# Optimization experiments

Hardware: AMD Instinct MI355X
Metric: run time of the kernel (lower is better)

Reference implementation:

```python
import jax, jax.numpy as jnp
import numpy as np

N = 50000        # nodes
E = 800000       # edges (before self-loops)
IN = 512         # in_channels
HEADS = 8        # 'head' arg: heads and per-head out dim of conv1
C1 = 8           # per-head channels of conv1 (== head)
OUT = 128        # out_channels of conv2
NEG_SLOPE = 0.2  # PyG GATConv leaky-relu slope


def _glorot(key, shape, fan_in):
    return jax.random.normal(key, shape, jnp.float32) * (1.0 / np.sqrt(fan_in))


def setup_inputs() -> dict:
    key = jax.random.key(0)
    ks = jax.random.split(key, 10)
    x = jax.random.normal(ks[0], (N, IN), jnp.float32)
    edge_index = jax.random.randint(ks[1], (2, E), 0, N, dtype=jnp.int32)
    # conv1: GATConv(IN, C1, heads=HEADS, concat=True)
    W1 = _glorot(ks[2], (IN, HEADS * C1), IN)
    att_src1 = _glorot(ks[3], (HEADS, C1), C1)
    att_dst1 = _glorot(ks[4], (HEADS, C1), C1)
    bias1 = jnp.zeros((HEADS * C1,), jnp.float32)
    # conv2: GATConv(HEADS*C1, OUT, heads=1, concat=False)
    W2 = _glorot(ks[5], (HEADS * C1, OUT), HEADS * C1)
    att_src2 = _glorot(ks[6], (1, OUT), OUT)
    att_dst2 = _glorot(ks[7], (1, OUT), OUT)
    bias2 = jnp.zeros((OUT,), jnp.float32)
    return {"x": x, "edge_index": edge_index,
            "W1": W1, "att_src1": att_src1, "att_dst1": att_dst1, "bias1": bias1,
            "W2": W2, "att_src2": att_src2, "att_dst2": att_dst2, "bias2": bias2}


def gat_conv(x, src, dst, W, a_src, a_dst, bias, heads, concat):
    """PyG GATConv (eval mode, dropout off). src/dst already include self-loops."""
    n = x.shape[0]
    h = (x @ W).reshape(n, heads, -1)                 # [N, H, C]
    s = (h * a_src[None]).sum(-1)                     # [N, H] alpha_src per node
    d = (h * a_dst[None]).sum(-1)                     # [N, H] alpha_dst per node
    alpha = jax.nn.leaky_relu(s[src] + d[dst], NEG_SLOPE)  # [E, H]
    # segment softmax over incoming edges of each destination node
    amax = jax.ops.segment_max(alpha, dst, num_segments=n)  # [N, H]
    amax = jnp.where(jnp.isfinite(amax), amax, 0.0)
    ea = jnp.exp(alpha - amax[dst])                   # [E, H]
    denom = jax.ops.segment_sum(ea, dst, num_segments=n)
    w = ea / (denom[dst] + 1e-16)                     # [E, H]
    msg = h[src] * w[..., None]                       # [E, H, C]
    out = jax.ops.segment_sum(msg, dst, num_segments=n)  # [N, H, C]
    out = out.reshape(n, -1) if concat else out.mean(axis=1)
    return out + bias


def reference(x, edge_index, W1, att_src1, att_dst1, bias1,
              W2, att_src2, att_dst2, bias2):
    n = x.shape[0]
    loop = jnp.arange(n, dtype=edge_index.dtype)      # PyG adds self-loops
    src = jnp.concatenate([edge_index[0], loop])
    dst = jnp.concatenate([edge_index[1], loop])
    h = jax.nn.elu(gat_conv(x, src, dst, W1, att_src1, att_dst1, bias1,
                            heads=HEADS, concat=True))
    out = jax.nn.elu(gat_conv(h, src, dst, W2, att_src2, att_dst2, bias2,
                              heads=1, concat=False))
    return out
```

## Files before the change

kernel.cpp:

```cpp
#include <hip/hip_runtime.h>

#define NEG_SLOPE 0.2f
#define CAP 128

typedef __attribute__((ext_vector_type(8))) short bf16x8;
typedef __attribute__((ext_vector_type(4))) float f32x4;

__device__ __forceinline__ float leaky(float v) {
    return v > 0.0f ? v : NEG_SLOPE * v;
}
__device__ __forceinline__ float elu(float v) {
    return v > 0.0f ? v : (__expf(v) - 1.0f);
}
__device__ __forceinline__ short f2b(float f) {
    return (short)((__float_as_uint(f) + 0x8000u) >> 16);
}
__device__ __forceinline__ float bf2f(unsigned short v) {
    return __uint_as_float(((unsigned)v) << 16);
}

__global__ void prep_k(const float* __restrict__ W1, const float* __restrict__ W2,
                       unsigned short* __restrict__ w1s, unsigned short* __restrict__ w2s,
                       int* __restrict__ wp, int N) {
    int i = blockIdx.x * 256 + threadIdx.x;
    if (i < N) wp[i] = 0;
    if (i < 512 * 64) {
        int k = i >> 6, n = i & 63;
        int kt = k >> 5, kk = k & 31;
        int nt = n >> 4, nn = n & 15;
        int lane = (kk >> 3) * 16 + nn, j = kk & 7;
        w1s[(((size_t)(kt * 4 + nt)) * 64 + lane) * 8 + j] = (unsigned short)f2b(W1[i]);
    } else if (i < 512 * 64 + 64 * 128) {
        int i2 = i - 512 * 64;
        int k = i2 >> 7, n = i2 & 127;
        int kt = k >> 5, kk = k & 31;
        int nt = n >> 4, nn = n & 15;
        int lane = (kk >> 3) * 16 + nn, j = kk & 7;
        w2s[(((size_t)(kt * 8 + nt)) * 64 + lane) * 8 + j] = (unsigned short)f2b(W2[i2]);
    }
}

__global__ __launch_bounds__(256) void g1pack_k(const float* __restrict__ X,
                                                const unsigned short* __restrict__ Ws,
                                                const float* __restrict__ Asrc,
                                                const float* __restrict__ Adst,
                                                unsigned short* __restrict__ Hb,
                                                float* __restrict__ S,
                                                float* __restrict__ D,
                                                const int* __restrict__ ei, int E,
                                                int* __restrict__ wp,
                                                int* __restrict__ srcs,
                                                int N, int gblk) {
    if ((int)blockIdx.x >= gblk) {
        int e = ((int)blockIdx.x - gblk) * 256 + threadIdx.x;
        if (e < E) {
            int s = ei[e];
            int d = ei[E + e];
            int c = atomicAdd(&wp[d], 1);
            if (c < CAP) srcs[((size_t)d << 7) + c] = s;
        }
        return;
    }
    const int lane = threadIdx.x & 63;
    const int wave = threadIdx.x >> 6;
    const int m0 = blockIdx.x * 64 + wave * 16;
    const int q = lane >> 4, lc = lane & 15;
    const int arow = m0 + lc;
    const float* xrow = X + (size_t)min(arow, N - 1) * 512 + q * 8;
    const bf16x8* bW = (const bf16x8*)Ws;

    f32x4 acc[4] = {{0.f,0.f,0.f,0.f},{0.f,0.f,0.f,0.f},{0.f,0.f,0.f,0.f},{0.f,0.f,0.f,0.f}};

    for (int g = 0; g < 2; ++g) {
        float4 a[16];
#pragma unroll
        for (int u = 0; u < 16; ++u)
            a[u] = *(const float4*)(xrow + g * 256 + (u >> 1) * 32 + (u & 1) * 4);
#pragma unroll
        for (int u2 = 0; u2 < 8; ++u2) {
            const int kt = g * 8 + u2;
            float4 a0 = a[u2 * 2], a1 = a[u2 * 2 + 1];
            bf16x8 af;
            af[0] = f2b(a0.x); af[1] = f2b(a0.y); af[2] = f2b(a0.z); af[3] = f2b(a0.w);
            af[4] = f2b(a1.x); af[5] = f2b(a1.y); af[6] = f2b(a1.z); af[7] = f2b(a1.w);
#pragma unroll
            for (int nt = 0; nt < 4; ++nt) {
                bf16x8 bf = bW[(size_t)(kt * 4 + nt) * 64 + lane];
                acc[nt] = __builtin_amdgcn_mfma_f32_16x16x32_bf16(af, bf, acc[nt], 0, 0, 0);
            }
        }
    }

    float asc[4], adc[4];
#pragma unroll
    for (int nt = 0; nt < 4; ++nt) { asc[nt] = Asrc[nt * 16 + lc]; adc[nt] = Adst[nt * 16 + lc]; }

#pragma unroll
    for (int r = 0; r < 4; ++r) {
        int row = m0 + q * 4 + r;
        bool ok = row < N;
        if (ok) {
#pragma unroll
            for (int nt = 0; nt < 4; ++nt)
                Hb[(size_t)row * 64 + nt * 16 + lc] = (unsigned short)f2b(acc[nt][r]);
        }
        float ps[4], pd[4];
#pragma unroll
        for (int nt = 0; nt < 4; ++nt) { ps[nt] = acc[nt][r] * asc[nt]; pd[nt] = acc[nt][r] * adc[nt]; }
#pragma unroll
        for (int off = 1; off < 8; off <<= 1) {
#pragma unroll
            for (int nt = 0; nt < 4; ++nt) {
                ps[nt] += __shfl_xor(ps[nt], off);
                pd[nt] += __shfl_xor(pd[nt], off);
            }
        }
        if (ok && !(lc & 7)) {
            int hb = lc >> 3;
#pragma unroll
            for (int nt = 0; nt < 4; ++nt) {
                S[(size_t)row * 8 + nt * 2 + hb] = ps[nt];
                D[(size_t)row * 8 + nt * 2 + hb] = pd[nt];
            }
        }
    }
}

__global__ __launch_bounds__(256) void agg1g2_k(const int* __restrict__ wp,
                                                const int* __restrict__ srcs,
                                                const float* __restrict__ S1,
                                                const float* __restrict__ D1,
                                                const unsigned short* __restrict__ H1b,
                                                const float* __restrict__ b1,
                                                const unsigned short* __restrict__ W2s,
                                                const float* __restrict__ as2,
                                                const float* __restrict__ ad2,
                                                unsigned short* __restrict__ H2b,
                                                float* __restrict__ S2,
                                                float* __restrict__ D2, int N) {
    __shared__ unsigned short sh[16][64];
    __shared__ float shp[4][16], shq[4][16];

    const int tid  = threadIdx.x;
    const int lane = tid & 63;
    const int wave = tid >> 6;
    const int m0 = blockIdx.x * 16;

    const int h = lane & 7;
    const int eg = lane >> 3;
#pragma unroll
    for (int rep = 0; rep < 4; ++rep) {
        const int nl = wave * 4 + rep;
        const int wid = m0 + nl;
        if (wid < N) {
            const int deg = min(wp[wid], CAP);
            const size_t b0 = (size_t)wid << 7;
            const float dvh = D1[(size_t)wid * 8 + h];

            float wself = __expf(leaky(S1[(size_t)wid * 8 + h] + dvh));
            float den = (eg == 0) ? wself : 0.0f;
            float acc[8] = {0.f,0.f,0.f,0.f,0.f,0.f,0.f,0.f};
            if (eg == 0) {
                bf16x8 hv = *(const bf16x8*)(H1b + (size_t)wid * 64 + h * 8);
#pragma unroll
                for (int c = 0; c < 8; ++c)
                    acc[c] = wself * bf2f((unsigned short)hv[c]);
            }

            for (int base = 0; base < deg; base += 8) {
                int i = base + eg;
                bool v = i < deg;
                int src = v ? srcs[b0 + i] : wid;
                float w = v ? __expf(leaky(S1[(size_t)src * 8 + h] + dvh)) : 0.0f;
                den += w;
                bf16x8 hv = *(const bf16x8*)(H1b + (size_t)src * 64 + h * 8);
#pragma unroll
                for (int c = 0; c < 8; ++c)
                    acc[c] += w * bf2f((unsigned short)hv[c]);
            }
#pragma unroll
            for (int off = 8; off < 64; off <<= 1) {
                den += __shfl_xor(den, off);
#pragma unroll
                for (int c = 0; c < 8; ++c)
                    acc[c] += __shfl_xor(acc[c], off);
            }
            if (eg == 0) {
                const float rden = 1.0f / (den + 1e-16f);
                bf16x8 o;
#pragma unroll
                for (int c = 0; c < 8; ++c)
                    o[c] = f2b(elu(acc[c] * rden + b1[h * 8 + c]));
                *(bf16x8*)(&sh[nl][h * 8]) = o;
            }
        } else if (eg == 0) {
            *(bf16x8*)(&sh[nl][h * 8]) = bf16x8{0,0,0,0,0,0,0,0};
        }
    }
    __syncthreads();

    const int q = lane >> 4, lc = lane & 15;
    const bf16x8* bW = (const bf16x8*)W2s;
    const int nt0 = wave * 2;

    f32x4 acc2[2] = {{0.f,0.f,0.f,0.f},{0.f,0.f,0.f,0.f}};
#pragma unroll
    for (int kt = 0; kt < 2; ++kt) {
        bf16x8 af = *(const bf16x8*)(&sh[lc][q * 8 + kt * 32]);
#pragma unroll
        for (int u = 0; u < 2; ++u) {
            bf16x8 bf = bW[(size_t)(kt * 8 + nt0 + u) * 64 + lane];
            acc2[u] = __builtin_amdgcn_mfma_f32_16x16x32_bf16(af, bf, acc2[u], 0, 0, 0);
        }
    }
    float asc[2], adc[2];
#pragma unroll
    for (int u = 0; u < 2; ++u) {
        asc[u] = as2[(nt0 + u) * 16 + lc];
        adc[u] = ad2[(nt0 + u) * 16 + lc];
    }
#pragma unroll
    for (int r = 0; r < 4; ++r) {
        int rl = q * 4 + r;
        int row = m0 + rl;
        if (row < N) {
#pragma unroll
            for (int u = 0; u < 2; ++u)
                H2b[(size_t)row * 128 + (nt0 + u) * 16 + lc] = (unsigned short)f2b(acc2[u][r]);
        }
        float ps = acc2[0][r] * asc[0] + acc2[1][r] * asc[1];
        float pd = acc2[0][r] * adc[0] + acc2[1][r] * adc[1];
#pragma unroll
        for (int off = 1; off < 16; off <<= 1) {
            ps += __shfl_xor(ps, off);
            pd += __shfl_xor(pd, off);
        }
        if (lc == 0) { shp[wave][rl] = ps; shq[wave][rl] = pd; }
    }
    __syncthreads();
    if (tid < 16) {
        int row = m0 + tid;
        if (row < N) {
            float s = shp[0][tid] + shp[1][tid] + shp[2][tid] + shp[3][tid];
            float d = shq[0][tid] + shq[1][tid] + shq[2][tid] + shq[3][tid];
            S2[row] = s;
            D2[row] = d;
        }
    }
}

__global__ __launch_bounds__(256) void agg2_k(const int* __restrict__ wp,
                                              const int* __restrict__ srcs,
                                              const float* __restrict__ S,
                                              const float* __restrict__ D,
                                              const unsigned short* __restrict__ Hb,
                                              const float* __restrict__ bias,
                                              float* __restrict__ out, int N) {
    const int wid = (blockIdx.x * 256 + threadIdx.x) >> 6;
    const int lane = threadIdx.x & 63;
    if (wid >= N) return;
    const int deg = min(wp[wid], CAP);
    const size_t b0 = (size_t)wid << 7;
    const float dv = D[wid];
    const int eg = lane >> 3;
    const int sl = lane & 7;
    const int c0 = sl * 16;

    const float wself = __expf(leaky(S[wid] + dv));
    float den = (eg == 0) ? wself : 0.0f;
    float acc[16] = {0.f,0.f,0.f,0.f,0.f,0.f,0.f,0.f,
                     0.f,0.f,0.f,0.f,0.f,0.f,0.f,0.f};
    if (eg == 0) {
        bf16x8 hv0 = *(const bf16x8*)(Hb + (size_t)wid * 128 + c0);
        bf16x8 hv1 = *(const bf16x8*)(Hb + (size_t)wid * 128 + c0 + 8);
#pragma unroll
        for (int c = 0; c < 8; ++c) {
            acc[c]     = wself * bf2f((unsigned short)hv0[c]);
            acc[c + 8] = wself * bf2f((unsigned short)hv1[c]);
        }
    }

    for (int base = 0; base < deg; base += 8) {
        int i = base + eg;
        bool v = i < deg;
        int src = v ? srcs[b0 + i] : wid;
        float w = v ? __expf(leaky(S[src] + dv)) : 0.0f;
        den += w;
        bf16x8 hv0 = *(const bf16x8*)(Hb + (size_t)src * 128 + c0);
        bf16x8 hv1 = *(const bf16x8*)(Hb + (size_t)src * 128 + c0 + 8);
#pragma unroll
        for (int c = 0; c < 8; ++c) {
            acc[c]     += w * bf2f((unsigned short)hv0[c]);
            acc[c + 8] += w * bf2f((unsigned short)hv1[c]);
        }
    }
#pragma unroll
    for (int off = 1; off < 64; off <<= 1)
        den += __shfl_xor(den, off);
#pragma unroll
    for (int off = 8; off < 64; off <<= 1) {
#pragma unroll
        for (int c = 0; c < 16; ++c)
            acc[c] += __shfl_xor(acc[c], off);
    }
    if (eg == 0) {
        const float rden = 1.0f / (den * 0.125f + 1e-16f);
        float4 o[4];
#pragma unroll
        for (int u = 0; u < 4; ++u) {
            o[u].x = elu(acc[u * 4 + 0] * rden + bias[c0 + u * 4 + 0]);
            o[u].y = elu(acc[u * 4 + 1] * rden + bias[c0 + u * 4 + 1]);
            o[u].z = elu(acc[u * 4 + 2] * rden + bias[c0 + u * 4 + 2]);
            o[u].w = elu(acc[u * 4 + 3] * rden + bias[c0 + u * 4 + 3]);
        }
#pragma unroll
        for (int u = 0; u < 4; ++u)
            *(float4*)(out + (size_t)wid * 128 + c0 + u * 4) = o[u];
    }
}

extern "C" void kernel_launch(void* const* d_in, const int* in_sizes, int n_in,
                              void* d_out, int out_size, void* d_ws, size_t ws_size,
                              hipStream_t stream) {
    const float* x   = (const float*)d_in[0];
    const int*   ei  = (const int*)d_in[1];
    const float* W1  = (const float*)d_in[2];
    const float* as1 = (const float*)d_in[3];
    const float* ad1 = (const float*)d_in[4];
    const float* b1  = (const float*)d_in[5];
    const float* W2  = (const float*)d_in[6];
    const float* as2 = (const float*)d_in[7];
    const float* ad2 = (const float*)d_in[8];
    const float* b2  = (const float*)d_in[9];

    const int N = in_sizes[0] / 512;
    const int E = in_sizes[1] / 2;

    unsigned short* w1s  = (unsigned short*)d_ws;
    unsigned short* w2s  = w1s + 512 * 64;
    unsigned short* h1b  = w2s + 64 * 128;
    unsigned short* h2b  = h1b + (size_t)N * 64;
    float*          s1   = (float*)(h2b + (size_t)N * 128);
    float*          d1   = s1 + (size_t)N * 8;
    float*          s2   = d1 + (size_t)N * 8;
    float*          d2   = s2 + N;
    int*            wp   = (int*)(d2 + N);
    int*            srcs = wp + N;

    const int B = 256;
    const int gblk  = (N + 63) / 64;
    const int packb = (E + B - 1) / B;
    int prep_n = 512 * 64 + 64 * 128;
    if (N > prep_n) prep_n = N;

    prep_k<<<(prep_n + B - 1) / B, B, 0, stream>>>(W1, W2, w1s, w2s, wp, N);
    g1pack_k<<<gblk + packb, B, 0, stream>>>(x, w1s, as1, ad1, h1b, s1, d1,
                                             ei, E, wp, srcs, N, gblk);
    agg1g2_k<<<(N + 15) / 16, B, 0, stream>>>(wp, srcs, s1, d1, h1b, b1,
                                              w2s, as2, ad2, h2b, s2, d2, N);
    agg2_k<<<(N + 3) / 4, B, 0, stream>>>(wp, srcs, s2, d2, h2b, b2,
                                          (float*)d_out, N);
}
```

Measured before the change: 309.6 us.

## Aggregate conv2 on 64-dim inputs before projecting with W2

Uses linearity to reorder the second GAT layer. The per-node attention scores come from precomputed vectors W2·a_src and W2·a_dst applied to the 64-dim layer-1 output. Edge aggregation then runs on 64-wide bf16 rows, and the W2 MFMA projection plus bias and ELU are applied after the softmax-weighted sum. This halves the gather width in the heavy second aggregation and drops the 128-wide H2 intermediate. The cost is a small serial dot-product loop in the prep kernel and some rounding differences, since the scores now come from bf16-rounded activations.

```diff
diff --git a/kernel.cpp b/kernel.cpp
--- a/kernel.cpp
+++ b/kernel.cpp
@@ -20,10 +20,21 @@
 }
 
 __global__ void prep_k(const float* __restrict__ W1, const float* __restrict__ W2,
+                       const float* __restrict__ as2, const float* __restrict__ ad2,
                        unsigned short* __restrict__ w1s, unsigned short* __restrict__ w2s,
+                       float* __restrict__ va, float* __restrict__ vd,
                        int* __restrict__ wp, int N) {
     int i = blockIdx.x * 256 + threadIdx.x;
     if (i < N) wp[i] = 0;
+    if (i < 64) {
+        float sa = 0.f, sd = 0.f;
+        for (int n = 0; n < 128; ++n) {
+            float w = W2[i * 128 + n];
+            sa += w * as2[n];
+            sd += w * ad2[n];
+        }
+        va[i] = sa; vd[i] = sd;
+    }
     if (i < 512 * 64) {
         int k = i >> 6, n = i & 63;
         int kt = k >> 5, kk = k & 31;
@@ -126,28 +137,99 @@
     }
 }
 
-__global__ __launch_bounds__(256) void agg1g2_k(const int* __restrict__ wp,
-                                                const int* __restrict__ srcs,
-                                                const float* __restrict__ S1,
-                                                const float* __restrict__ D1,
-                                                const unsigned short* __restrict__ H1b,
-                                                const float* __restrict__ b1,
-                                                const unsigned short* __restrict__ W2s,
-                                                const float* __restrict__ as2,
-                                                const float* __restrict__ ad2,
-                                                unsigned short* __restrict__ H2b,
-                                                float* __restrict__ S2,
-                                                float* __restrict__ D2, int N) {
-    __shared__ unsigned short sh[16][64];
-    __shared__ float shp[4][16], shq[4][16];
-
+__global__ __launch_bounds__(256) void agg1_k(const int* __restrict__ wp,
+                                              const int* __restrict__ srcs,
+                                              const float* __restrict__ S1,
+                                              const float* __restrict__ D1,
+                                              const unsigned short* __restrict__ H1b,
+                                              const float* __restrict__ b1,
+                                              const float* __restrict__ va,
+                                              const float* __restrict__ vd,
+                                              unsigned short* __restrict__ A1b,
+                                              float* __restrict__ S2,
+                                              float* __restrict__ D2, int N) {
     const int tid  = threadIdx.x;
     const int lane = tid & 63;
     const int wave = tid >> 6;
     const int m0 = blockIdx.x * 16;
-
     const int h = lane & 7;
     const int eg = lane >> 3;
+
+#pragma unroll
+    for (int rep = 0; rep < 4; ++rep) {
+        const int wid = m0 + wave * 4 + rep;
+        if (wid >= N) continue;
+        const int deg = min(wp[wid], CAP);
+        const size_t b0 = (size_t)wid << 7;
+        const float dvh = D1[(size_t)wid * 8 + h];
+
+        float wself = __expf(leaky(S1[(size_t)wid * 8 + h] + dvh));
+        float den = (eg == 0) ? wself : 0.0f;
+        float acc[8] = {0.f,0.f,0.f,0.f,0.f,0.f,0.f,0.f};
+        if (eg == 0) {
+            bf16x8 hv = *(const bf16x8*)(H1b + (size_t)wid * 64 + h * 8);
+#pragma unroll
+            for (int c = 0; c < 8; ++c)
+                acc[c] = wself * bf2f((unsigned short)hv[c]);
+        }
+
+        for (int base = 0; base < deg; base += 8) {
+            int i = base + eg;
+            bool v = i < deg;
+            int src = v ? srcs[b0 + i] : wid;
+            float w = v ? __expf(leaky(S1[(size_t)src * 8 + h] + dvh)) : 0.0f;
+            den += w;
+            bf16x8 hv = *(const bf16x8*)(H1b + (size_t)src * 64 + h * 8);
+#pragma unroll
+            for (int c = 0; c < 8; ++c)
+                acc[c] += w * bf2f((unsigned short)hv[c]);
+        }
+#pragma unroll
+        for (int off = 8; off < 64; off <<= 1) {
+            den += __shfl_xor(den, off);
+#pragma unroll
+            for (int c = 0; c < 8; ++c)
+                acc[c] += __shfl_xor(acc[c], off);
+        }
+        const float rden = 1.0f / (den + 1e-16f);
+        bf16x8 o;
+        float ps = 0.f, pd = 0.f;
+#pragma unroll
+        for (int c = 0; c < 8; ++c) {
+            float fv = elu(acc[c] * rden + b1[h * 8 + c]);
+            o[c] = f2b(fv);
+            float fr = bf2f((unsigned short)o[c]);
+            ps += fr * va[h * 8 + c];
+            pd += fr * vd[h * 8 + c];
+        }
+        if (eg == 0)
+            *(bf16x8*)(A1b + (size_t)wid * 64 + h * 8) = o;
+#pragma unroll
+        for (int off = 1; off < 8; off <<= 1) {
+            ps += __shfl_xor(ps, off);
+            pd += __shfl_xor(pd, off);
+        }
+        if (lane == 0) { S2[wid] = ps; D2[wid] = pd; }
+    }
+}
+
+__global__ __launch_bounds__(256) void agg2g2_k(const int* __restrict__ wp,
+                                                const int* __restrict__ srcs,
+                                                const float* __restrict__ S2,
+                                                const float* __restrict__ D2,
+                                                const unsigned short* __restrict__ A1b,
+                                                const unsigned short* __restrict__ W2s,
+                                                const float* __restrict__ b2,
+                                                float* __restrict__ out, int N) {
+    __shared__ unsigned short sh[16][64];
+
+    const int tid  = threadIdx.x;
+    const int lane = tid & 63;
+    const int wave = tid >> 6;
+    const int m0 = blockIdx.x * 16;
+    const int sl = lane & 7;
+    const int eg = lane >> 3;
+
 #pragma unroll
     for (int rep = 0; rep < 4; ++rep) {
         const int nl = wave * 4 + rep;
@@ -155,13 +237,13 @@
         if (wid < N) {
             const int deg = min(wp[wid], CAP);
             const size_t b0 = (size_t)wid << 7;
-            const float dvh = D1[(size_t)wid * 8 + h];
-
-            float wself = __expf(leaky(S1[(size_t)wid * 8 + h] + dvh));
+            const float dv = D2[wid];
+
+            const float wself = __expf(leaky(S2[wid] + dv));
             float den = (eg == 0) ? wself : 0.0f;
             float acc[8] = {0.f,0.f,0.f,0.f,0.f,0.f,0.f,0.f};
             if (eg == 0) {
-                bf16x8 hv = *(const bf16x8*)(H1b + (size_t)wid * 64 + h * 8);
+                bf16x8 hv = *(const bf16x8*)(A1b + (size_t)wid * 64 + sl * 8);
 #pragma unroll
                 for (int c = 0; c < 8; ++c)
                     acc[c] = wself * bf2f((unsigned short)hv[c]);
@@ -171,30 +253,32 @@
                 int i = base + eg;
                 bool v = i < deg;
                 int src = v ? srcs[b0 + i] : wid;
-                float w = v ? __expf(leaky(S1[(size_t)src * 8 + h] + dvh)) : 0.0f;
+                float w = v ? __expf(leaky(S2[src] + dv)) : 0.0f;
                 den += w;
-                bf16x8 hv = *(const bf16x8*)(H1b + (size_t)src * 64 + h * 8);
+                bf16x8 hv = *(const bf16x8*)(A1b + (size_t)src * 64 + sl * 8);
 #pragma unroll
                 for (int c = 0; c < 8; ++c)
                     acc[c] += w * bf2f((unsigned short)hv[c]);
             }
 #pragma unroll
+            for (int off = 1; off < 64; off <<= 1)
+                den += __shfl_xor(den, off);
+#pragma unroll
             for (int off = 8; off < 64; off <<= 1) {
-                den += __shfl_xor(den, off);
 #pragma unroll
                 for (int c = 0; c < 8; ++c)
                     acc[c] += __shfl_xor(acc[c], off);
             }
             if (eg == 0) {
-                const float rden = 1.0f / (den + 1e-16f);
+                const float rden = 1.0f / (den * 0.125f + 1e-16f);
                 bf16x8 o;
 #pragma unroll
                 for (int c = 0; c < 8; ++c)
-                    o[c] = f2b(elu(acc[c] * rden + b1[h * 8 + c]));
-                *(bf16x8*)(&sh[nl][h * 8]) = o;
+                    o[c] = f2b(acc[c] * rden);
+                *(bf16x8*)(&sh[nl][sl * 8]) = o;
             }
         } else if (eg == 0) {
-            *(bf16x8*)(&sh[nl][h * 8]) = bf16x8{0,0,0,0,0,0,0,0};
+            *(bf16x8*)(&sh[nl][sl * 8]) = bf16x8{0,0,0,0,0,0,0,0};
         }
     }
     __syncthreads();
@@ -212,12 +296,6 @@
             bf16x8 bf = bW[(size_t)(kt * 8 + nt0 + u) * 64 + lane];
             acc2[u] = __builtin_amdgcn_mfma_f32_16x16x32_bf16(af, bf, acc2[u], 0, 0, 0);
         }
-    }
-    float asc[2], adc[2];
-#pragma unroll
-    for (int u = 0; u < 2; ++u) {
-        asc[u] = as2[(nt0 + u) * 16 + lc];
-        adc[u] = ad2[(nt0 + u) * 16 + lc];
     }
 #pragma unroll
     for (int r = 0; r < 4; ++r) {
@@ -225,97 +303,11 @@
         int row = m0 + rl;
         if (row < N) {
 #pragma unroll
-            for (int u = 0; u < 2; ++u)
-                H2b[(size_t)row * 128 + (nt0 + u) * 16 + lc] = (unsigned short)f2b(acc2[u][r]);
-        }
-        float ps = acc2[0][r] * asc[0] + acc2[1][r] * asc[1];
-        float pd = acc2[0][r] * adc[0] + acc2[1][r] * adc[1];
-#pragma unroll
-        for (int off = 1; off < 16; off <<= 1) {
-            ps += __shfl_xor(ps, off);
-            pd += __shfl_xor(pd, off);
-        }
-        if (lc == 0) { shp[wave][rl] = ps; shq[wave][rl] = pd; }
-    }
-    __syncthreads();
-    if (tid < 16) {
-        int row = m0 + tid;
-        if (row < N) {
-            float s = shp[0][tid] + shp[1][tid] + shp[2][tid] + shp[3][tid];
-            float d = shq[0][tid] + shq[1][tid] + shq[2][tid] + shq[3][tid];
-            S2[row] = s;
-            D2[row] = d;
-        }
-    }
-}
-
-__global__ __launch_bounds__(256) void agg2_k(const int* __restrict__ wp,
-                                              const int* __restrict__ srcs,
-                                              const float* __restrict__ S,
-                                              const float* __restrict__ D,
-                                              const unsigned short* __restrict__ Hb,
-                                              const float* __restrict__ bias,
-                                              float* __restrict__ out, int N) {
-    const int wid = (blockIdx.x * 256 + threadIdx.x) >> 6;
-    const int lane = threadIdx.x & 63;
-    if (wid >= N) return;
-    const int deg = min(wp[wid], CAP);
-    const size_t b0 = (size_t)wid << 7;
-    const float dv = D[wid];
-    const int eg = lane >> 3;
-    const int sl = lane & 7;
-    const int c0 = sl * 16;
-
-    const float wself = __expf(leaky(S[wid] + dv));
-    float den = (eg == 0) ? wself : 0.0f;
-    float acc[16] = {0.f,0.f,0.f,0.f,0.f,0.f,0.f,0.f,
-                     0.f,0.f,0.f,0.f,0.f,0.f,0.f,0.f};
-    if (eg == 0) {
-        bf16x8 hv0 = *(const bf16x8*)(Hb + (size_t)wid * 128 + c0);
-        bf16x8 hv1 = *(const bf16x8*)(Hb + (size_t)wid * 128 + c0 + 8);
-#pragma unroll
-        for (int c = 0; c < 8; ++c) {
-            acc[c]     = wself * bf2f((unsigned short)hv0[c]);
-            acc[c + 8] = wself * bf2f((unsigned short)hv1[c]);
-        }
-    }
-
-    for (int base = 0; base < deg; base += 8) {
-        int i = base + eg;
-        bool v = i < deg;
-        int src = v ? srcs[b0 + i] : wid;
-        float w = v ? __expf(leaky(S[src] + dv)) : 0.0f;
-        den += w;
-        bf16x8 hv0 = *(const bf16x8*)(Hb + (size_t)src * 128 + c0);
-        bf16x8 hv1 = *(const bf16x8*)(Hb + (size_t)src * 128 + c0 + 8);
-#pragma unroll
-        for (int c = 0; c < 8; ++c) {
-            acc[c]     += w * bf2f((unsigned short)hv0[c]);
-            acc[c + 8] += w * bf2f((unsigned short)hv1[c]);
-        }
-    }
-#pragma unroll
-    for (int off = 1; off < 64; off <<= 1)
-        den += __shfl_xor(den, off);
-#pragma unroll
-    for (int off = 8; off < 64; off <<= 1) {
-#pragma unroll
-        for (int c = 0; c < 16; ++c)
-            acc[c] += __shfl_xor(acc[c], off);
-    }
-    if (eg == 0) {
-        const float rden = 1.0f / (den * 0.125f + 1e-16f);
-        float4 o[4];
-#pragma unroll
-        for (int u = 0; u < 4; ++u) {
-            o[u].x = elu(acc[u * 4 + 0] * rden + bias[c0 + u * 4 + 0]);
-            o[u].y = elu(acc[u * 4 + 1] * rden + bias[c0 + u * 4 + 1]);
-            o[u].z = elu(acc[u * 4 + 2] * rden + bias[c0 + u * 4 + 2]);
-            o[u].w = elu(acc[u * 4 + 3] * rden + bias[c0 + u * 4 + 3]);
-        }
-#pragma unroll
-        for (int u = 0; u < 4; ++u)
-            *(float4*)(out + (size_t)wid * 128 + c0 + u * 4) = o[u];
+            for (int u = 0; u < 2; ++u) {
+                int col = (nt0 + u) * 16 + lc;
+                out[(size_t)row * 128 + col] = elu(acc2[u][r] + b2[col]);
+            }
+        }
     }
 }
 
@@ -339,12 +331,14 @@
     unsigned short* w1s  = (unsigned short*)d_ws;
     unsigned short* w2s  = w1s + 512 * 64;
     unsigned short* h1b  = w2s + 64 * 128;
-    unsigned short* h2b  = h1b + (size_t)N * 64;
-    float*          s1   = (float*)(h2b + (size_t)N * 128);
+    unsigned short* a1b  = h1b + (size_t)N * 64;
+    float*          s1   = (float*)(a1b + (size_t)N * 64);
     float*          d1   = s1 + (size_t)N * 8;
     float*          s2   = d1 + (size_t)N * 8;
     float*          d2   = s2 + N;
-    int*            wp   = (int*)(d2 + N);
+    float*          va   = d2 + N;
+    float*          vd   = va + 64;
+    int*            wp   = (int*)(vd + 64);
     int*            srcs = wp + N;
 
     const int B = 256;
@@ -353,11 +347,12 @@
     int prep_n = 512 * 64 + 64 * 128;
     if (N > prep_n) prep_n = N;
 
-    prep_k<<<(prep_n + B - 1) / B, B, 0, stream>>>(W1, W2, w1s, w2s, wp, N);
+    prep_k<<<(prep_n + B - 1) / B, B, 0, stream>>>(W1, W2, as2, ad2, w1s, w2s,
+                                                   va, vd, wp, N);
     g1pack_k<<<gblk + packb, B, 0, stream>>>(x, w1s, as1, ad1, h1b, s1, d1,
                                              ei, E, wp, srcs, N, gblk);
-    agg1g2_k<<<(N + 15) / 16, B, 0, stream>>>(wp, srcs, s1, d1, h1b, b1,
-                                              w2s, as2, ad2, h2b, s2, d2, N);
-    agg2_k<<<(N + 3) / 4, B, 0, stream>>>(wp, srcs, s2, d2, h2b, b2,
-                                          (float*)d_out, N);
-}
+    agg1_k<<<(N + 15) / 16, B, 0, stream>>>(wp, srcs, s1, d1, h1b, b1,
+                                            va, vd, a1b, s2, d2, N);
+    agg2g2_k<<<(N + 15) / 16, B, 0, stream>>>(wp, srcs, s2, d2, a1b,
+                                              w2s, b2, (float*)d_out, N);
+}
```

Measured after the change: 309.2 us. No clear change (-0.1%).
